# Optimization experiments

Hardware: AMD Instinct MI355X
Metric: run time of the kernel (lower is better)

## Reference

```python
import jax, jax.numpy as jnp
import numpy as np

B, T, C = 4, 4096, 1024   # batch, seq_len, n_embd
HS = 128                  # tamanho_cabeca (head size)


def setup_inputs() -> dict:
    key = jax.random.key(0)
    kx, kq, kk, kv = jax.random.split(key, 4)
    scale = 0.02
    return {
        "x": jax.random.normal(kx, (B, T, C), dtype=jnp.float32),
        "Wq": jax.random.normal(kq, (C, HS), dtype=jnp.float32) * scale,
        "Wk": jax.random.normal(kk, (C, HS), dtype=jnp.float32) * scale,
        "Wv": jax.random.normal(kv, (C, HS), dtype=jnp.float32) * scale,
    }


def reference(x, Wq, Wk, Wv):
    # Single-head causal self-attention, faithful to the torch Head module.
    _, Tn, Cn = x.shape
    q = jnp.einsum("btc,ch->bth", x, Wq)
    k = jnp.einsum("btc,ch->bth", x, Wk)
    v = jnp.einsum("btc,ch->bth", x, Wv)
    # NOTE: original scales by C**-0.5 (input embed dim), not head_size**-0.5.
    scores = jnp.einsum("bth,bsh->bts", q, k) * (Cn ** -0.5)
    causal = jnp.tril(jnp.ones((Tn, Tn), dtype=bool))  # [T, T]
    scores = jnp.where(causal, scores, -jnp.inf)
    probs = jax.nn.softmax(scores, axis=-1)
    return jnp.einsum("bts,bsh->bth", probs, v)
```

## Files before the change

### kernel.cpp

```cpp
#include <hip/hip_runtime.h>
#include <hip/hip_bf16.h>
#include <math.h>

typedef __attribute__((ext_vector_type(8))) short short8;
typedef __attribute__((ext_vector_type(4))) float f32x4;
typedef unsigned short ushort_t;

#define B_  4
#define T_  4096
#define C_  1024
#define HS_ 128

#define QSCALE 0.04508422002778011f

__device__ const unsigned char NS_[32] = {
    1,1,1,2,2,2,3,3,3,4,4,4,5,5,5,6,6,7,7,7,8,8,8,9,9,9,10,10,11,11,10,11};

__device__ __forceinline__ ushort_t f2bf(float f) {
    unsigned int u = __float_as_uint(f);
    u = (u + 0x7FFFu + ((u >> 16) & 1u)) >> 16;
    return (ushort_t)u;
}
__device__ __forceinline__ ushort_t f2bf_fast(float f) {
    return (ushort_t)((__float_as_uint(f) + 0x8000u) >> 16);
}
__device__ __forceinline__ float bf2f(ushort_t u) {
    return __uint_as_float(((unsigned)u) << 16);
}
__device__ __forceinline__ void async16(const void* g, void* l) {
    __builtin_amdgcn_global_load_lds(
        (const __attribute__((address_space(1))) unsigned int*)g,
        (__attribute__((address_space(3))) unsigned int*)l, 16, 0, 0);
}
__device__ __forceinline__ float exp2fast(float x) {
    return __builtin_amdgcn_exp2f(x);
}
__device__ __forceinline__ void stnt8(ushort_t* p, short8 v) {
    __builtin_nontemporal_store(v, (short8*)p);
}

__global__ __launch_bounds__(256) void wt_kernel(
    const float* __restrict__ Wq, const float* __restrict__ Wk,
    const float* __restrict__ Wv, ushort_t* __restrict__ WT3)
{
    __shared__ ushort_t sWT[128 * 68];
    const int blk = blockIdx.x, tid = threadIdx.x;
    const int m = blk >> 4, slab = blk & 15;
    const float* __restrict__ W = (m == 0) ? Wq : (m == 1) ? Wk : Wv;
    const int kc = slab * 64;
    const int r = tid >> 2, h0 = (tid & 3) * 32;
#pragma unroll
    for (int j = 0; j < 8; ++j) {
        float4 wv = *(const float4*)(W + (size_t)(kc + r) * 128 + h0 + j * 4);
        sWT[(h0 + j * 4 + 0) * 68 + r] = f2bf(wv.x);
        sWT[(h0 + j * 4 + 1) * 68 + r] = f2bf(wv.y);
        sWT[(h0 + j * 4 + 2) * 68 + r] = f2bf(wv.z);
        sWT[(h0 + j * 4 + 3) * 68 + r] = f2bf(wv.w);
    }
    __syncthreads();
#pragma unroll
    for (int j = 0; j < 4; ++j) {
        int d = j * 256 + tid;
        int h = d >> 3, c8 = d & 7;
        short8 o;
#pragma unroll
        for (int e = 0; e < 8; ++e) o[e] = (short)sWT[h * 68 + c8 * 8 + e];
        *(short8*)(WT3 + (size_t)(m * 128 + h) * 1024 + kc + c8 * 8) = o;
    }
}

__global__ __launch_bounds__(256, 3) void qkv_gemm(
    const float* __restrict__ x, const ushort_t* __restrict__ WT3,
    ushort_t* __restrict__ q, ushort_t* __restrict__ k,
    ushort_t* __restrict__ vT)
{
    __shared__ ushort_t smem[24576];

    const int tid  = threadIdx.x;
    const int t0   = blockIdx.x * 64;
    const int mm   = blockIdx.y;
    const int w    = tid >> 6, lane = tid & 63;
    const int quad = lane >> 4, l15 = lane & 15;

    const ushort_t* __restrict__ WTm = WT3 + (size_t)mm * (128 * 1024);

    const int arow = tid >> 3, ac = tid & 7;
    const float* __restrict__ gx = x + (size_t)(t0 + arow) * C_ + ac * 8;
    const int aswz = ((ac ^ (arow & 7)) * 8);

    const ushort_t* gB[4];
    int bdst[4];
#pragma unroll
    for (int j = 0; j < 4; ++j) {
        int d = j * 256 + tid, row = d >> 3, c = d & 7;
        gB[j] = WTm + (size_t)row * C_ + ((c ^ (row & 7)) * 8);
        bdst[j] = 4096 + d * 8;
    }

    f32x4 acc[8];
#pragma unroll
    for (int nt = 0; nt < 8; ++nt) acc[nt] = (f32x4)0.f;

    float4 ar[2][2];
#pragma unroll
    for (int p = 0; p < 2; ++p) {
        ar[p][0] = *(const float4*)(gx + (size_t)(p * 32) * C_);
        ar[p][1] = *(const float4*)(gx + (size_t)(p * 32) * C_ + 4);
    }
#pragma unroll
    for (int j = 0; j < 4; ++j) async16(gB[j], &smem[bdst[j]]);
#pragma unroll
    for (int p = 0; p < 2; ++p) {
        short8 sv;
        sv[0]=f2bf(ar[p][0].x); sv[1]=f2bf(ar[p][0].y);
        sv[2]=f2bf(ar[p][0].z); sv[3]=f2bf(ar[p][0].w);
        sv[4]=f2bf(ar[p][1].x); sv[5]=f2bf(ar[p][1].y);
        sv[6]=f2bf(ar[p][1].z); sv[7]=f2bf(ar[p][1].w);
        *(short8*)&smem[(p * 32 + arow) * 64 + aswz] = sv;
    }
    __syncthreads();

    const int arow_q = w * 16 + l15;
    for (int it = 0; it < 16; ++it) {
        const int buf = it & 1, nb = buf ^ 1;
        const bool more = (it < 15);
        if (more) {
            const int kc = (it + 1) * 64;
#pragma unroll
            for (int p = 0; p < 2; ++p) {
                ar[p][0] = *(const float4*)(gx + (size_t)(p * 32) * C_ + kc);
                ar[p][1] = *(const float4*)(gx + (size_t)(p * 32) * C_ + kc + 4);
            }
#pragma unroll
            for (int j = 0; j < 4; ++j)
                async16(gB[j] + kc, &smem[nb * 12288 + bdst[j]]);
        }
        const ushort_t* sA = &smem[buf * 12288];
        const ushort_t* sB = &smem[buf * 12288 + 4096];
#pragma unroll
        for (int kf = 0; kf < 2; ++kf) {
            short8 af = *(const short8*)&sA[arow_q * 64 + (((kf * 4 + quad) ^ (arow_q & 7)) * 8)];
#pragma unroll
            for (int nt = 0; nt < 8; ++nt) {
                int row = nt * 16 + l15;
                short8 bf = *(const short8*)&sB[row * 64 + (((kf * 4 + quad) ^ (row & 7)) * 8)];
                acc[nt] = __builtin_amdgcn_mfma_f32_16x16x32_bf16(af, bf, acc[nt], 0, 0, 0);
            }
        }
        if (more) {
#pragma unroll
            for (int p = 0; p < 2; ++p) {
                short8 sv;
                sv[0]=f2bf(ar[p][0].x); sv[1]=f2bf(ar[p][0].y);
                sv[2]=f2bf(ar[p][0].z); sv[3]=f2bf(ar[p][0].w);
                sv[4]=f2bf(ar[p][1].x); sv[5]=f2bf(ar[p][1].y);
                sv[6]=f2bf(ar[p][1].z); sv[7]=f2bf(ar[p][1].w);
                *(short8*)&smem[nb * 12288 + (p * 32 + arow) * 64 + aswz] = sv;
            }
        }
        __syncthreads();
    }

    if (mm < 2) {
        ushort_t* __restrict__ outp = (mm == 0) ? q : k;
        const float s = (mm == 0) ? QSCALE : 1.0f;
        ushort_t* sE = &smem[0];
#pragma unroll
        for (int nt = 0; nt < 8; ++nt)
#pragma unroll
            for (int rr = 0; rr < 4; ++rr)
                sE[(w * 16 + quad * 4 + rr) * 136 + nt * 16 + l15] =
                    f2bf(acc[nt][rr] * s);
        __syncthreads();
#pragma unroll
        for (int j = 0; j < 4; ++j) {
            int d = j * 256 + tid;
            int row = d >> 4, cs = d & 15;
            *(short8*)(outp + (size_t)(t0 + row) * HS_ + cs * 8) =
                *(const short8*)&sE[row * 136 + cs * 8];
        }
    } else {
        ushort_t* sT = &smem[0];
#pragma unroll
        for (int nt = 0; nt < 8; ++nt)
#pragma unroll
            for (int rr = 0; rr < 4; ++rr)
                sT[(w * 16 + quad * 4 + rr) * 132 + nt * 16 + l15] =
                    f2bf(acc[nt][rr]);
        __syncthreads();
        const int bb = t0 >> 12;
        const int tl = t0 & (T_ - 1);
#pragma unroll
        for (int j = 0; j < 4; ++j) {
            int d = j * 256 + tid;
            int h = d >> 3, t8 = d & 7;
            short8 o;
#pragma unroll
            for (int e = 0; e < 8; ++e)
                o[e] = (short)sT[(t8 * 8 + e) * 132 + h];
            *(short8*)(vT + ((size_t)(bb * HS_) + h) * T_ + tl + t8 * 8) = o;
        }
    }
}

__global__ __launch_bounds__(256, 3) void attn_seg(
    const ushort_t* __restrict__ q, const ushort_t* __restrict__ k,
    const ushort_t* __restrict__ vT, ushort_t* __restrict__ Opart,
    float* __restrict__ lseg)
{
    __shared__ ushort_t smem[23552];
    ushort_t* sKb = smem;
    ushort_t* sVb = smem + 8192;
    ushort_t* sP  = smem + 18432;

    const int tid  = threadIdx.x;
    const int bid  = blockIdx.x;
    const int bb   = (bid & 7) >> 1;
    const int seg  = ((bid >> 3) << 1) | (bid & 1);
    const int slot = bb * 192 + seg;
    int r_ = seg;
    int i = 0;
    while (r_ >= NS_[i]) { r_ -= NS_[i]; ++i; }
    const int s    = r_;
    const int ns   = NS_[i];
    const int qb   = i << 7;
    const int nkc  = (i + 1) << 2;
    const int c0   = (nkc * s) / ns;
    const int c1   = (nkc * (s + 1)) / ns;

    const int w    = tid >> 6, lane = tid & 63;
    const int quad = lane >> 4, l15 = lane & 15;
    const size_t bT = (size_t)bb << 12;

    const int kr0 = tid >> 4,          kc0 = tid & 15;
    const int kr1 = (tid + 256) >> 4,  kc1 = (tid + 256) & 15;
    const ushort_t* kp0 = k + (bT + (size_t)c0 * 32 + kr0) * HS_ + ((kc0 ^ (kr0 & 15)) * 8);
    const ushort_t* kp1 = k + (bT + (size_t)c0 * 32 + kr1) * HS_ + ((kc1 ^ (kr1 & 15)) * 8);
    const int vr0 = tid >> 2,          vc0 = tid & 3;
    const int vr1 = (tid + 256) >> 2,  vc1 = (tid + 256) & 3;
    const ushort_t* vp0 = vT + ((size_t)(bb * HS_) + vr0) * T_ + c0 * 32 + vc0 * 8;
    const ushort_t* vp1 = vT + ((size_t)(bb * HS_) + vr1) * T_ + c0 * 32 + vc1 * 8;
    const int vdst0 = vr0 * 40 + vc0 * 8;
    const int vdst1 = vr1 * 40 + vc1 * 8;

    short8 qf[2][4];
#pragma unroll
    for (int mt = 0; mt < 2; ++mt)
#pragma unroll
        for (int kf = 0; kf < 4; ++kf)
            qf[mt][kf] = *(const short8*)(
                q + (bT + qb + w * 32 + mt * 16 + l15) * HS_ + kf * 32 + quad * 8);

    f32x4 O[2][8];
    f32x4 O_l[2];
#pragma unroll
    for (int mt = 0; mt < 2; ++mt) {
        O_l[mt] = (f32x4)0.f;
#pragma unroll
        for (int nt = 0; nt < 8; ++nt) O[mt][nt] = (f32x4)0.f;
    }
    short8 ones;
#pragma unroll
    for (int e = 0; e < 8; ++e) ones[e] = (short)0x3F80;

    {
        short8 v0 = *(const short8*)vp0;
        short8 v1 = *(const short8*)vp1;
        async16(kp0, sKb + tid * 8);
        async16(kp1, sKb + (tid + 256) * 8);
        kp0 += 32 * HS_; kp1 += 32 * HS_; vp0 += 32; vp1 += 32;
        *(short8*)(sVb + vdst0) = v0;
        *(short8*)(sVb + vdst1) = v1;
    }
    __syncthreads();

    for (int c = c0; c < c1; ++c) {
        const int buf = (c - c0) & 1, nb = buf ^ 1;
        const int kb = c << 5;
        const bool more = (c + 1 < c1);
        short8 pv0, pv1;
        if (more) {
            pv0 = *(const short8*)vp0;
            pv1 = *(const short8*)vp1;
            async16(kp0, sKb + nb * 4096 + tid * 8);
            async16(kp1, sKb + nb * 4096 + (tid + 256) * 8);
            kp0 += 32 * HS_; kp1 += 32 * HS_; vp0 += 32; vp1 += 32;
        }
        const ushort_t* sK = sKb + buf * 4096;
        const ushort_t* sV = sVb + buf * 5120;

        f32x4 S[2][2];
        S[0][0] = (f32x4)0.f; S[0][1] = (f32x4)0.f;
        S[1][0] = (f32x4)0.f; S[1][1] = (f32x4)0.f;
#pragma unroll
        for (int nt = 0; nt < 2; ++nt) {
            int row = nt * 16 + l15;
#pragma unroll
            for (int kf = 0; kf < 4; ++kf) {
                short8 bf = *(const short8*)&sK[row * 128 + (((kf * 4 + quad) ^ l15) * 8)];
                S[0][nt] = __builtin_amdgcn_mfma_f32_16x16x32_bf16(qf[0][kf], bf, S[0][nt], 0, 0, 0);
                S[1][nt] = __builtin_amdgcn_mfma_f32_16x16x32_bf16(qf[1][kf], bf, S[1][nt], 0, 0, 0);
            }
        }
        if (kb + 31 > qb + w * 32) {
#pragma unroll
            for (int mt = 0; mt < 2; ++mt)
#pragma unroll
                for (int nt = 0; nt < 2; ++nt)
#pragma unroll
                    for (int rr = 0; rr < 4; ++rr)
                        if (kb + nt * 16 + l15 > qb + w * 32 + mt * 16 + quad * 4 + rr)
                            S[mt][nt][rr] = -1e30f;
        }
#pragma unroll
        for (int mt = 0; mt < 2; ++mt)
#pragma unroll
            for (int nt = 0; nt < 2; ++nt)
#pragma unroll
                for (int rr = 0; rr < 4; ++rr)
                    sP[w * 1280 + (mt * 16 + quad * 4 + rr) * 40 + nt * 16 + l15] =
                        f2bf_fast(exp2fast(S[mt][nt][rr]));
#pragma unroll
        for (int mt = 0; mt < 2; ++mt) {
            short8 pf = *(short8*)&sP[w * 1280 + (mt * 16 + l15) * 40 + quad * 8];
            O_l[mt] = __builtin_amdgcn_mfma_f32_16x16x32_bf16(pf, ones, O_l[mt], 0, 0, 0);
#pragma unroll
            for (int nt = 0; nt < 8; ++nt) {
                short8 vf = *(const short8*)&sV[(nt * 16 + l15) * 40 + quad * 8];
                O[mt][nt] = __builtin_amdgcn_mfma_f32_16x16x32_bf16(pf, vf, O[mt][nt], 0, 0, 0);
            }
        }
        if (more) {
            *(short8*)(sVb + nb * 5120 + vdst0) = pv0;
            *(short8*)(sVb + nb * 5120 + vdst1) = pv1;
        }
        __syncthreads();
    }

    ushort_t* sE = smem;
#pragma unroll
    for (int mt = 0; mt < 2; ++mt)
#pragma unroll
        for (int nt = 0; nt < 8; ++nt)
#pragma unroll
            for (int rr = 0; rr < 4; ++rr)
                sE[(w * 32 + mt * 16 + quad * 4 + rr) * 136 + nt * 16 + l15] =
                    f2bf(O[mt][nt][rr]);
    if (l15 == 0)
#pragma unroll
        for (int mt = 0; mt < 2; ++mt)
#pragma unroll
            for (int rr = 0; rr < 4; ++rr)
                lseg[slot * 128 + w * 32 + mt * 16 + quad * 4 + rr] = O_l[mt][rr];
    __syncthreads();
#pragma unroll
    for (int j = 0; j < 8; ++j) {
        int d = j * 256 + tid;
        int row = d >> 4, cs = d & 15;
        stnt8(Opart + (size_t)slot * 16384 + row * 128 + cs * 8,
              *(const short8*)&sE[row * 136 + cs * 8]);
    }
}

__global__ __launch_bounds__(256) void combine_kernel(
    const ushort_t* __restrict__ Opart, const float* __restrict__ lseg,
    float* __restrict__ out)
{
    const int blk  = blockIdx.x;
    const int tile = blk >> 3, rg = blk & 7;
    const int i    = tile & 31;
    int sb = (tile >> 5) * 192;
    for (int j = 0; j < i; ++j) sb += NS_[j];
    const int ns  = NS_[i];
    const int row = rg * 16 + (threadIdx.x >> 4);
    const int col = (threadIdx.x & 15) * 8;

    const ushort_t* op = Opart + (size_t)sb * 16384 + row * 128 + col;
    const float*    lp = lseg + sb * 128 + row;

    float den = lp[0];
    short8 cur = *(const short8*)op;
    float acc[8];
#pragma unroll
    for (int e = 0; e < 8; ++e) acc[e] = 0.f;
    for (int s = 1; s < ns; ++s) {
        short8 nxt = *(const short8*)(op + (size_t)s * 16384);
        float  dn  = lp[s * 128];
#pragma unroll
        for (int e = 0; e < 8; ++e) acc[e] += bf2f((ushort_t)cur[e]);
        den += dn;
        cur = nxt;
    }
#pragma unroll
    for (int e = 0; e < 8; ++e) acc[e] += bf2f((ushort_t)cur[e]);

    const float inv = 1.0f / den;
    float* o = out + ((size_t)tile * 128 + row) * 128 + col;
    float4 v0 = make_float4(acc[0] * inv, acc[1] * inv, acc[2] * inv, acc[3] * inv);
    float4 v1 = make_float4(acc[4] * inv, acc[5] * inv, acc[6] * inv, acc[7] * inv);
    *(float4*)o = v0;
    *(float4*)(o + 4) = v1;
}

extern "C" void kernel_launch(void* const* d_in, const int* in_sizes, int n_in,
                              void* d_out, int out_size, void* d_ws, size_t ws_size,
                              hipStream_t stream)
{
    const float* x  = (const float*)d_in[0];
    const float* Wq = (const float*)d_in[1];
    const float* Wk = (const float*)d_in[2];
    const float* Wv = (const float*)d_in[3];
    float* out = (float*)d_out;

    ushort_t* WT3 = (ushort_t*)d_ws;
    ushort_t* q   = WT3 + 393216;
    ushort_t* k   = q + 2097152;
    ushort_t* vT  = k + 2097152;
    ushort_t* Opart = vT + 2097152;
    float* lseg   = (float*)(Opart + 768 * 16384);

    wt_kernel<<<48, 256, 0, stream>>>(Wq, Wk, Wv, WT3);
    qkv_gemm<<<dim3(256, 3), 256, 0, stream>>>(x, WT3, q, k, vT);
    attn_seg<<<768, 256, 0, stream>>>(q, k, vT, Opart, lseg);
    combine_kernel<<<1024, 256, 0, stream>>>(Opart, lseg, out);
}
```

Baseline: 170.9 us.

## Triple-buffer K tiles with two-ahead prefetch and XOR-swizzle V shared layout

K tiles move from double to triple buffering in shared memory, with async loads issued two chunks ahead. The full __syncthreads is replaced by an explicit s_waitcnt vmcnt(4) plus barrier, so in-flight prefetches can stay outstanding across iterations. V register-staged loads are also issued a chunk earlier, and the V shared tile changes from a padded stride-40 layout to a dense stride-32 XOR-swizzled one to avoid bank conflicts. This raises LDS use, which may lower occupancy, and the vmcnt accounting is fragile.

Measured after the change: 174.0 us. About the same (+1.8%).

```diff
diff --git a/kernel.cpp b/kernel.cpp
--- a/kernel.cpp
+++ b/kernel.cpp
@@ -208,10 +208,10 @@
     const ushort_t* __restrict__ vT, ushort_t* __restrict__ Opart,
     float* __restrict__ lseg)
 {
-    __shared__ ushort_t smem[23552];
+    __shared__ ushort_t smem[25600];
     ushort_t* sKb = smem;
-    ushort_t* sVb = smem + 8192;
-    ushort_t* sP  = smem + 18432;
+    ushort_t* sVb = smem + 12288;
+    ushort_t* sP  = smem + 20480;
 
     const int tid  = threadIdx.x;
     const int bid  = blockIdx.x;
@@ -240,8 +240,8 @@
     const int vr1 = (tid + 256) >> 2,  vc1 = (tid + 256) & 3;
     const ushort_t* vp0 = vT + ((size_t)(bb * HS_) + vr0) * T_ + c0 * 32 + vc0 * 8;
     const ushort_t* vp1 = vT + ((size_t)(bb * HS_) + vr1) * T_ + c0 * 32 + vc1 * 8;
-    const int vdst0 = vr0 * 40 + vc0 * 8;
-    const int vdst1 = vr1 * 40 + vc1 * 8;
+    const int vdst0 = vr0 * 32 + ((vc0 ^ (vr0 & 3)) * 8);
+    const int vdst1 = vr1 * 32 + ((vc1 ^ (vr1 & 3)) * 8);
 
     short8 qf[2][4];
 #pragma unroll
@@ -263,31 +263,49 @@
 #pragma unroll
     for (int e = 0; e < 8; ++e) ones[e] = (short)0x3F80;
 
+    int rK = c0 % 3;
+    int vb = 0;
+    short8 pv0, pv1;
+
     {
         short8 v0 = *(const short8*)vp0;
         short8 v1 = *(const short8*)vp1;
-        async16(kp0, sKb + tid * 8);
-        async16(kp1, sKb + (tid + 256) * 8);
+        async16(kp0, sKb + rK * 4096 + tid * 8);
+        async16(kp1, sKb + rK * 4096 + (tid + 256) * 8);
         kp0 += 32 * HS_; kp1 += 32 * HS_; vp0 += 32; vp1 += 32;
         *(short8*)(sVb + vdst0) = v0;
         *(short8*)(sVb + vdst1) = v1;
-    }
-    __syncthreads();
-
-    for (int c = c0; c < c1; ++c) {
-        const int buf = (c - c0) & 1, nb = buf ^ 1;
-        const int kb = c << 5;
-        const bool more = (c + 1 < c1);
-        short8 pv0, pv1;
-        if (more) {
+        if (c0 + 1 < c1) {
             pv0 = *(const short8*)vp0;
             pv1 = *(const short8*)vp1;
-            async16(kp0, sKb + nb * 4096 + tid * 8);
-            async16(kp1, sKb + nb * 4096 + (tid + 256) * 8);
+            int k1 = (rK == 2) ? 0 : rK + 1;
+            async16(kp0, sKb + k1 * 4096 + tid * 8);
+            async16(kp1, sKb + k1 * 4096 + (tid + 256) * 8);
             kp0 += 32 * HS_; kp1 += 32 * HS_; vp0 += 32; vp1 += 32;
         }
-        const ushort_t* sK = sKb + buf * 4096;
-        const ushort_t* sV = sVb + buf * 5120;
+        asm volatile("s_waitcnt vmcnt(4) lgkmcnt(0)" ::: "memory");
+        __builtin_amdgcn_s_barrier();
+    }
+
+    for (int c = c0; c < c1; ++c) {
+        const int kb = c << 5;
+        const bool haveNext = (c + 1 < c1);
+        const bool havePf   = (c + 2 < c1);
+
+        if (haveNext) {
+            *(short8*)(sVb + (vb ^ 1) * 4096 + vdst0) = pv0;
+            *(short8*)(sVb + (vb ^ 1) * 4096 + vdst1) = pv1;
+        }
+        if (havePf) {
+            pv0 = *(const short8*)vp0;
+            pv1 = *(const short8*)vp1;
+            int wK = rK + 2; if (wK >= 3) wK -= 3;
+            async16(kp0, sKb + wK * 4096 + tid * 8);
+            async16(kp1, sKb + wK * 4096 + (tid + 256) * 8);
+            kp0 += 32 * HS_; kp1 += 32 * HS_; vp0 += 32; vp1 += 32;
+        }
+        const ushort_t* sK = sKb + rK * 4096;
+        const ushort_t* sV = sVb + vb * 4096;
 
         f32x4 S[2][2];
         S[0][0] = (f32x4)0.f; S[0][1] = (f32x4)0.f;
@@ -326,15 +344,15 @@
             O_l[mt] = __builtin_amdgcn_mfma_f32_16x16x32_bf16(pf, ones, O_l[mt], 0, 0, 0);
 #pragma unroll
             for (int nt = 0; nt < 8; ++nt) {
-                short8 vf = *(const short8*)&sV[(nt * 16 + l15) * 40 + quad * 8];
+                int rv = nt * 16 + l15;
+                short8 vf = *(const short8*)&sV[rv * 32 + ((quad ^ (rv & 3)) * 8)];
                 O[mt][nt] = __builtin_amdgcn_mfma_f32_16x16x32_bf16(pf, vf, O[mt][nt], 0, 0, 0);
             }
         }
-        if (more) {
-            *(short8*)(sVb + nb * 5120 + vdst0) = pv0;
-            *(short8*)(sVb + nb * 5120 + vdst1) = pv1;
-        }
-        __syncthreads();
+        asm volatile("s_waitcnt vmcnt(4) lgkmcnt(0)" ::: "memory");
+        __builtin_amdgcn_s_barrier();
+        rK = (rK == 2) ? 0 : rK + 1;
+        vb ^= 1;
     }
 
     ushort_t* sE = smem;
```
